# Kernel optimization log

Hardware: AMD Instinct MI355X
Metric: run time of the kernel (lower is better)

## Reference

```python
import jax, jax.numpy as jnp
import numpy as np

B, H, S, D = 2, 16, 2048, 64

def setup_inputs() -> dict:
    key = jax.random.key(0)
    kq, kk, kv, km = jax.random.split(key, 4)
    q = jax.random.normal(kq, (B, H, S, D), dtype=jnp.float32)
    k = jax.random.normal(kk, (B, H, S, D), dtype=jnp.float32)
    v = jax.random.normal(kv, (B, H, S, D), dtype=jnp.float32)
    mask = jax.random.randint(km, (B, 1, S, S), 0, 2, dtype=jnp.int32)
    return {"q": q, "k": k, "v": v, "mask": mask}

def reference(q, k, v, mask):
    d_model = q.shape[-1]
    # scores: [B, H, S, S]
    score = jnp.einsum('bhqd,bhkd->bhqk', q, k) / jnp.sqrt(jnp.float32(d_model))
    score = jnp.where(mask == 0, jnp.float32(-1e9), score)
    attn = jax.nn.softmax(score, axis=-1)
    return jnp.einsum('bhqk,bhkd->bhqd', attn, v)
```

## Files before the change

### kernel.cpp

```cpp
#include <hip/hip_runtime.h>
#include <hip/hip_bf16.h>


#define B_ 2
#define H_ 16
#define S_ 2048
#define D_ 64
#define BQ 128
#define NW 4
#define BK 64
#define NT (S_ / BK)
#define PADW 72
#define TILEB (BK * D_ * 2)

typedef __attribute__((ext_vector_type(4))) float f32x4;
typedef __attribute__((ext_vector_type(8))) short bf16x8;
typedef __attribute__((ext_vector_type(4))) short bf16x4;

#define QSCALE 0.1803368801111137f
#define MASKNEG (-1.4426950408889634e9f)

static __device__ __forceinline__ short f2bf(float f) {
  __hip_bfloat16 h = __float2bfloat16(f);
  short s; __builtin_memcpy(&s, &h, sizeof(s)); return s;
}
static __device__ __forceinline__ float fexp2(float x) {
  return __builtin_amdgcn_exp2f(x);
}
static __device__ __forceinline__ unsigned cvt_pk_bf16(float a, float b) {
  unsigned r;
  asm("v_cvt_pk_bf16_f32 %0, %1, %2" : "=v"(r) : "v"(a), "v"(b));
  return r;
}
static __device__ __forceinline__ void gload_lds16(const void* g, void* l) {
  __builtin_amdgcn_global_load_lds(
      (__attribute__((address_space(1))) void*)g,
      (__attribute__((address_space(3))) void*)l, 16, 0, 0);
}

__global__ __launch_bounds__(256)
void pack_all(const float* __restrict__ kg, const float* __restrict__ vg,
              const int* __restrict__ mg,
              short* __restrict__ kw, short* __restrict__ vw,
              unsigned long long* __restrict__ mwp) {
  __shared__ float sv[BK][D_ + 1];
  const int bx  = blockIdx.x;
  const int tid = threadIdx.x;

  if (bx < 1024) {
    const int t  = bx & 31;
    const int bh = bx >> 5;
    const float* kt = kg + ((size_t)bh * S_ + t * BK) * D_;
    const float* vt = vg + ((size_t)bh * S_ + t * BK) * D_;
    short* ko = kw + ((size_t)bh * NT + t) * (BK * D_);
    short* vo = vw + ((size_t)bh * NT + t) * (BK * D_);

    const int row = tid >> 2;
    const int swz = (row & 7) << 4;

    #pragma unroll
    for (int c = 0; c < 2; ++c) {
      const int x = (tid & 3) * 32 + c * 16;
      const int dsrc = (x ^ swz) >> 1;
      const float4 u0 = *(const float4*)(kt + row * D_ + dsrc);
      const float4 u1 = *(const float4*)(kt + row * D_ + dsrc + 4);
      uint4 w;
      w.x = cvt_pk_bf16(u0.x, u0.y); w.y = cvt_pk_bf16(u0.z, u0.w);
      w.z = cvt_pk_bf16(u1.x, u1.y); w.w = cvt_pk_bf16(u1.z, u1.w);
      *(uint4*)(ko + row * D_ + (x >> 1)) = w;
    }

    #pragma unroll
    for (int i = 0; i < 4; ++i) {
      const int id = tid + 256 * i;
      const int r = id >> 4, c4 = (id & 15) * 4;
      const float4 u = *(const float4*)(vt + r * D_ + c4);
      sv[r][c4] = u.x; sv[r][c4+1] = u.y; sv[r][c4+2] = u.z; sv[r][c4+3] = u.w;
    }
    __syncthreads();
    #pragma unroll
    for (int c = 0; c < 2; ++c) {
      const int x = (tid & 3) * 32 + c * 16;
      const int ksrc = (x ^ swz) >> 1;
      uint4 w;
      w.x = cvt_pk_bf16(sv[ksrc+0][row], sv[ksrc+1][row]);
      w.y = cvt_pk_bf16(sv[ksrc+2][row], sv[ksrc+3][row]);
      w.z = cvt_pk_bf16(sv[ksrc+4][row], sv[ksrc+5][row]);
      w.w = cvt_pk_bf16(sv[ksrc+6][row], sv[ksrc+7][row]);
      *(uint4*)(vo + row * D_ + (x >> 1)) = w;
    }
  } else {
    const int r4   = bx - 1024;
    const int wv   = tid >> 6;
    const int lane = tid & 63;
    const int row  = r4 * 4 + wv;
    const int* mr = mg + (size_t)row * S_;
    unsigned long long* out = mwp + (size_t)row * NT;
    #pragma unroll
    for (int g = 0; g < 8; ++g) {
      const int4 v = *(const int4*)(mr + g * 256 + lane * 4);
      const unsigned long long b0 = __ballot(v.x != 0);
      const unsigned long long b1 = __ballot(v.y != 0);
      const unsigned long long b2 = __ballot(v.z != 0);
      const unsigned long long b3 = __ballot(v.w != 0);
      if (lane < 4) {
        const int tl = lane;
        const unsigned long long u =
            ((b0 >> (16 * tl)) & 0xFFFFULL)
          | (((b1 >> (16 * tl)) & 0xFFFFULL) << 16)
          | (((b2 >> (16 * tl)) & 0xFFFFULL) << 32)
          | (((b3 >> (16 * tl)) & 0xFFFFULL) << 48);
        out[g * 4 + tl] = u;
      }
    }
  }
}

static __device__ __forceinline__ float softmax_group(
    const f32x4* st, unsigned long long m64, int quad, char* spg,
    int l15, int swz) {
  const unsigned xlo = ((unsigned)m64) >> quad;
  const unsigned xhi = ((unsigned)(m64 >> 32)) >> quad;
  float l = 0.f;
  #pragma unroll
  for (int mt = 0; mt < 4; ++mt) {
    float p0 = fexp2(st[mt].x);
    float p1 = fexp2(st[mt].y);
    float p2 = fexp2(st[mt].z);
    float p3 = fexp2(st[mt].w);
    const int a0 = __builtin_amdgcn_sbfe((int)xlo, mt*4,      1);
    const int a1 = __builtin_amdgcn_sbfe((int)xlo, mt*4 + 16, 1);
    const int a2 = __builtin_amdgcn_sbfe((int)xhi, mt*4,      1);
    const int a3 = __builtin_amdgcn_sbfe((int)xhi, mt*4 + 16, 1);
    p0 = __uint_as_float(__float_as_uint(p0) & (unsigned)a0);
    p1 = __uint_as_float(__float_as_uint(p1) & (unsigned)a1);
    p2 = __uint_as_float(__float_as_uint(p2) & (unsigned)a2);
    p3 = __uint_as_float(__float_as_uint(p3) & (unsigned)a3);
    l += (p0 + p1) + (p2 + p3);
    uint2 uu;
    uu.x = cvt_pk_bf16(p0, p1);
    uu.y = cvt_pk_bf16(p2, p3);
    *(uint2*)(spg + l15*128 + ((mt*32 + quad*8) ^ swz)) = uu;
  }
  return l;
}

__global__ __launch_bounds__(256, 3)
void attn_main(const float* __restrict__ qg, const short* __restrict__ kw,
               const short* __restrict__ vw,
               const unsigned long long* __restrict__ mw,
               float* __restrict__ outg) {
  __shared__ short sKV[2][2][BK * D_];
  __shared__ short sP[NW][2][16][64];

  const int tid  = threadIdx.x;
  const int lane = tid & 63;
  const int wv   = tid >> 6;
  const int l15  = lane & 15;
  const int quad = lane >> 4;

  const int f  = blockIdx.y * 16 + blockIdx.x;
  const int nf = (f & 7) * 64 + (f >> 3);
  const int bh = nf >> 4;
  const int b  = bh >> 4;
  const int q0 = (nf & 15) * BQ;
  const int qw0 = q0 + wv * 32 + l15;
  const int qw1 = qw0 + 16;

  bf16x8 qf[2][2];
  #pragma unroll
  for (int g = 0; g < 2; ++g) {
    const float* qrow = qg + ((size_t)bh * S_ + (g ? qw1 : qw0)) * D_;
    #pragma unroll
    for (int ks = 0; ks < 2; ++ks) {
      const float4 u0 = *(const float4*)(qrow + ks*32 + quad*8);
      const float4 u1 = *(const float4*)(qrow + ks*32 + quad*8 + 4);
      bf16x8 fq;
      fq[0]=f2bf(u0.x*QSCALE); fq[1]=f2bf(u0.y*QSCALE);
      fq[2]=f2bf(u0.z*QSCALE); fq[3]=f2bf(u0.w*QSCALE);
      fq[4]=f2bf(u1.x*QSCALE); fq[5]=f2bf(u1.y*QSCALE);
      fq[6]=f2bf(u1.z*QSCALE); fq[7]=f2bf(u1.w*QSCALE);
      qf[g][ks] = fq;
    }
  }

  f32x4 O0[4], O1[4];
  #pragma unroll
  for (int dt = 0; dt < 4; ++dt) {
    O0[dt] = (f32x4){0.f, 0.f, 0.f, 0.f};
    O1[dt] = (f32x4){0.f, 0.f, 0.f, 0.f};
  }
  float la = 0.f, lb = 0.f;

  const char* kt = (const char*)(kw + (size_t)bh * NT * BK * D_);
  const char* vt = (const char*)(vw + (size_t)bh * NT * BK * D_);
  const unsigned long long* mb0 = mw + ((size_t)b * S_ + qw0) * NT;
  const unsigned long long* mb1 = mb0 + (size_t)16 * NT;
  const int so = tid * 16;

  const int swz = (l15 & 7) << 4;
  const int ro0 = l15*128 + (( 0 + quad*16) ^ swz);
  const int ro1 = l15*128 + ((64 + quad*16) ^ swz);
  char* const spw = (char*)sP + wv*4096;

  gload_lds16(kt + so,        (char*)sKV + so);
  gload_lds16(kt + 4096 + so, (char*)sKV + 4096 + so);
  gload_lds16(vt + so,        (char*)sKV + 8192 + so);
  gload_lds16(vt + 4096 + so, (char*)sKV + 12288 + so);
  kt += TILEB; vt += TILEB;
  int cur = 0;
  __syncthreads();

  for (int t = 0; t < NT; ++t) {
    const unsigned long long m64a = mb0[t];
    const unsigned long long m64b = mb1[t];
    if (t < NT - 1) {
      const int nb = (cur ^ 1) << 14;
      gload_lds16(kt + so,        (char*)sKV + nb + so);
      gload_lds16(kt + 4096 + so, (char*)sKV + nb + 4096 + so);
      gload_lds16(vt + so,        (char*)sKV + nb + 8192 + so);
      gload_lds16(vt + 4096 + so, (char*)sKV + nb + 12288 + so);
      kt += TILEB; vt += TILEB;
    }
    const char* kb = (const char*)sKV + (cur << 14);
    const char* vb = kb + 8192;

    f32x4 st0[4], st1[4];
    __builtin_amdgcn_s_setprio(1);
    #pragma unroll
    for (int mt = 0; mt < 4; ++mt) {
      const bf16x8 kf0 = *(const bf16x8*)(kb + mt*2048 + ro0);
      const bf16x8 kf1 = *(const bf16x8*)(kb + mt*2048 + ro1);
      f32x4 a0 = (f32x4){0.f, 0.f, 0.f, 0.f};
      f32x4 a1 = (f32x4){0.f, 0.f, 0.f, 0.f};
      a0 = __builtin_amdgcn_mfma_f32_16x16x32_bf16(kf0, qf[0][0], a0, 0, 0, 0);
      a1 = __builtin_amdgcn_mfma_f32_16x16x32_bf16(kf0, qf[1][0], a1, 0, 0, 0);
      a0 = __builtin_amdgcn_mfma_f32_16x16x32_bf16(kf1, qf[0][1], a0, 0, 0, 0);
      a1 = __builtin_amdgcn_mfma_f32_16x16x32_bf16(kf1, qf[1][1], a1, 0, 0, 0);
      st0[mt] = a0; st1[mt] = a1;
    }
    __builtin_amdgcn_s_setprio(0);

    la += softmax_group(st0, m64a, quad, spw,        l15, swz);
    lb += softmax_group(st1, m64b, quad, spw + 2048, l15, swz);

    asm volatile("s_waitcnt lgkmcnt(0)" ::: "memory");

    const bf16x8 pf00 = *(const bf16x8*)(spw +        l15*128 + (( 0 + quad*16) ^ swz));
    const bf16x8 pf01 = *(const bf16x8*)(spw +        l15*128 + ((64 + quad*16) ^ swz));
    const bf16x8 pf10 = *(const bf16x8*)(spw + 2048 + l15*128 + (( 0 + quad*16) ^ swz));
    const bf16x8 pf11 = *(const bf16x8*)(spw + 2048 + l15*128 + ((64 + quad*16) ^ swz));
    __builtin_amdgcn_s_setprio(1);
    #pragma unroll
    for (int dt = 0; dt < 4; ++dt) {
      const bf16x8 vf0 = *(const bf16x8*)(vb + dt*2048 + ro0);
      const bf16x8 vf1 = *(const bf16x8*)(vb + dt*2048 + ro1);
      O0[dt] = __builtin_amdgcn_mfma_f32_16x16x32_bf16(pf00, vf0, O0[dt], 0, 0, 0);
      O1[dt] = __builtin_amdgcn_mfma_f32_16x16x32_bf16(pf10, vf0, O1[dt], 0, 0, 0);
      O0[dt] = __builtin_amdgcn_mfma_f32_16x16x32_bf16(pf01, vf1, O0[dt], 0, 0, 0);
      O1[dt] = __builtin_amdgcn_mfma_f32_16x16x32_bf16(pf11, vf1, O1[dt], 0, 0, 0);
    }
    __builtin_amdgcn_s_setprio(0);

    __syncthreads();
    cur ^= 1;
  }

  la += __shfl_xor(la, 16);
  la += __shfl_xor(la, 32);
  lb += __shfl_xor(lb, 16);
  lb += __shfl_xor(lb, 32);
  float ira[4], irb[4];
  #pragma unroll
  for (int r = 0; r < 4; ++r) {
    ira[r] = 1.0f / __shfl(la, quad*4 + r);
    irb[r] = 1.0f / __shfl(lb, quad*4 + r);
  }

  float* ob0 = outg + ((size_t)bh * S_ + q0 + wv*32) * D_;
  float* ob1 = ob0 + 16 * D_;
  #pragma unroll
  for (int dt = 0; dt < 4; ++dt) {
    ob0[(quad*4 + 0)*D_ + dt*16 + l15] = O0[dt].x * ira[0];
    ob0[(quad*4 + 1)*D_ + dt*16 + l15] = O0[dt].y * ira[1];
    ob0[(quad*4 + 2)*D_ + dt*16 + l15] = O0[dt].z * ira[2];
    ob0[(quad*4 + 3)*D_ + dt*16 + l15] = O0[dt].w * ira[3];
    ob1[(quad*4 + 0)*D_ + dt*16 + l15] = O1[dt].x * irb[0];
    ob1[(quad*4 + 1)*D_ + dt*16 + l15] = O1[dt].y * irb[1];
    ob1[(quad*4 + 2)*D_ + dt*16 + l15] = O1[dt].z * irb[2];
    ob1[(quad*4 + 3)*D_ + dt*16 + l15] = O1[dt].w * irb[3];
  }
}

__global__ __launch_bounds__(256, 4)
void attn_fallback(const float* __restrict__ qg, const float* __restrict__ kg,
                   const float* __restrict__ vg, const int* __restrict__ maskg,
                   float* __restrict__ outg) {
  __shared__ short sK[BK][PADW];
  __shared__ short sVT[D_][PADW];
  __shared__ short sP[4][16][PADW];

  const int tid  = threadIdx.x;
  const int lane = tid & 63;
  const int wv   = tid >> 6;
  const int l15  = lane & 15;
  const int quad = lane >> 4;

  const int bh = blockIdx.y;
  const int b  = bh >> 4;
  const int q0 = blockIdx.x * 64;
  const int qw = q0 + wv * 16 + l15;

  bf16x8 qf[2];
  {
    const float* qrow = qg + ((size_t)bh * S_ + qw) * D_;
    #pragma unroll
    for (int ks = 0; ks < 2; ++ks) {
      const float4 u0 = *(const float4*)(qrow + ks*32 + quad*8);
      const float4 u1 = *(const float4*)(qrow + ks*32 + quad*8 + 4);
      bf16x8 fq;
      fq[0]=f2bf(u0.x*QSCALE); fq[1]=f2bf(u0.y*QSCALE);
      fq[2]=f2bf(u0.z*QSCALE); fq[3]=f2bf(u0.w*QSCALE);
      fq[4]=f2bf(u1.x*QSCALE); fq[5]=f2bf(u1.y*QSCALE);
      fq[6]=f2bf(u1.z*QSCALE); fq[7]=f2bf(u1.w*QSCALE);
      qf[ks] = fq;
    }
  }

  f32x4 O[4];
  #pragma unroll
  for (int dt = 0; dt < 4; ++dt) O[dt] = (f32x4){0.f, 0.f, 0.f, 0.f};
  float m = -3.0e38f, l = 0.f;

  const float* kbase = kg + (size_t)bh * S_ * D_;
  const float* vbase = vg + (size_t)bh * S_ * D_;
  const int*   mrow  = maskg + ((size_t)b * S_ + qw) * S_;

  for (int t0 = 0; t0 < S_; t0 += BK) {
    __syncthreads();
    #pragma unroll
    for (int i = 0; i < 4; ++i) {
      const int id = tid + 256*i;
      const int key = id >> 4, d4 = (id & 15) * 4;
      const float4 u = *(const float4*)(kbase + (size_t)(t0 + key)*D_ + d4);
      bf16x4 w; w[0]=f2bf(u.x); w[1]=f2bf(u.y); w[2]=f2bf(u.z); w[3]=f2bf(u.w);
      *(bf16x4*)&sK[key][d4] = w;
    }
    #pragma unroll
    for (int i = 0; i < 2; ++i) {
      const int id = tid + 256*i;
      const int kp = id & 31, d4 = (id >> 5) * 4;
      const float4 a = *(const float4*)(vbase + (size_t)(t0 + 2*kp    )*D_ + d4);
      const float4 c = *(const float4*)(vbase + (size_t)(t0 + 2*kp + 1)*D_ + d4);
      const float av[4] = {a.x, a.y, a.z, a.w};
      const float cv[4] = {c.x, c.y, c.z, c.w};
      #pragma unroll
      for (int j = 0; j < 4; ++j) {
        const unsigned pk = (unsigned)(unsigned short)f2bf(av[j])
                          | ((unsigned)(unsigned short)f2bf(cv[j]) << 16);
        *(unsigned*)&sVT[d4 + j][2*kp] = pk;
      }
    }
    __syncthreads();

    int4 mk[4];
    #pragma unroll
    for (int mt = 0; mt < 4; ++mt)
      mk[mt] = *(const int4*)(mrow + t0 + mt*16 + quad*4);

    f32x4 st[4];
    #pragma unroll
    for (int mt = 0; mt < 4; ++mt) {
      f32x4 acc = (f32x4){0.f, 0.f, 0.f, 0.f};
      #pragma unroll
      for (int ks = 0; ks < 2; ++ks) {
        const bf16x8 kf = *(const bf16x8*)&sK[mt*16 + l15][ks*32 + quad*8];
        acc = __builtin_amdgcn_mfma_f32_16x16x32_bf16(kf, qf[ks], acc, 0, 0, 0);
      }
      st[mt] = acc;
    }

    float cmax = -3.0e38f;
    #pragma unroll
    for (int mt = 0; mt < 4; ++mt) {
      f32x4 s = st[mt];
      s.x = mk[mt].x ? s.x : MASKNEG;
      s.y = mk[mt].y ? s.y : MASKNEG;
      s.z = mk[mt].z ? s.z : MASKNEG;
      s.w = mk[mt].w ? s.w : MASKNEG;
      st[mt] = s;
      cmax = fmaxf(cmax, fmaxf(fmaxf(s.x, s.y), fmaxf(s.z, s.w)));
    }
    cmax = fmaxf(cmax, __shfl_xor(cmax, 16));
    cmax = fmaxf(cmax, __shfl_xor(cmax, 32));
    const float mnew  = fmaxf(m, cmax);
    const float alpha = fexp2(m - mnew);
    m = mnew;

    float lsum = 0.f;
    #pragma unroll
    for (int mt = 0; mt < 4; ++mt) {
      const float p0 = fexp2(st[mt].x - mnew);
      const float p1 = fexp2(st[mt].y - mnew);
      const float p2 = fexp2(st[mt].z - mnew);
      const float p3 = fexp2(st[mt].w - mnew);
      lsum += (p0 + p1) + (p2 + p3);
      bf16x4 pw; pw[0]=f2bf(p0); pw[1]=f2bf(p1); pw[2]=f2bf(p2); pw[3]=f2bf(p3);
      *(bf16x4*)&sP[wv][l15][mt*16 + quad*4] = pw;
    }
    lsum += __shfl_xor(lsum, 16);
    lsum += __shfl_xor(lsum, 32);
    l = l * alpha + lsum;

    const float ar0 = __shfl(alpha, quad*4 + 0);
    const float ar1 = __shfl(alpha, quad*4 + 1);
    const float ar2 = __shfl(alpha, quad*4 + 2);
    const float ar3 = __shfl(alpha, quad*4 + 3);
    #pragma unroll
    for (int dt = 0; dt < 4; ++dt) {
      O[dt].x *= ar0; O[dt].y *= ar1; O[dt].z *= ar2; O[dt].w *= ar3;
    }

    asm volatile("s_waitcnt lgkmcnt(0)" ::: "memory");

    const bf16x8 pf0 = *(const bf16x8*)&sP[wv][l15][quad*8];
    const bf16x8 pf1 = *(const bf16x8*)&sP[wv][l15][32 + quad*8];
    #pragma unroll
    for (int dt = 0; dt < 4; ++dt) {
      const bf16x8 vf0 = *(const bf16x8*)&sVT[dt*16 + l15][quad*8];
      const bf16x8 vf1 = *(const bf16x8*)&sVT[dt*16 + l15][32 + quad*8];
      O[dt] = __builtin_amdgcn_mfma_f32_16x16x32_bf16(pf0, vf0, O[dt], 0, 0, 0);
      O[dt] = __builtin_amdgcn_mfma_f32_16x16x32_bf16(pf1, vf1, O[dt], 0, 0, 0);
    }
  }

  float ir[4];
  #pragma unroll
  for (int r = 0; r < 4; ++r) ir[r] = 1.0f / __shfl(l, quad*4 + r);

  float* ob = outg + ((size_t)bh * S_ + q0 + wv*16) * D_;
  #pragma unroll
  for (int dt = 0; dt < 4; ++dt) {
    ob[(quad*4 + 0)*D_ + dt*16 + l15] = O[dt].x * ir[0];
    ob[(quad*4 + 1)*D_ + dt*16 + l15] = O[dt].y * ir[1];
    ob[(quad*4 + 2)*D_ + dt*16 + l15] = O[dt].z * ir[2];
    ob[(quad*4 + 3)*D_ + dt*16 + l15] = O[dt].w * ir[3];
  }
}

extern "C" void kernel_launch(void* const* d_in, const int* in_sizes, int n_in,
                              void* d_out, int out_size, void* d_ws, size_t ws_size,
                              hipStream_t stream) {
  const float* q    = (const float*)d_in[0];
  const float* k    = (const float*)d_in[1];
  const float* v    = (const float*)d_in[2];
  const int*   mask = (const int*)d_in[3];
  float* out = (float*)d_out;

  const size_t kvbytes = (size_t)B_ * H_ * S_ * D_ * 2;
  const size_t mbytes  = (size_t)B_ * S_ * NT * 8;
  const size_t need    = 2 * kvbytes + mbytes;

  if (d_ws != nullptr && ws_size >= need) {
    short* kwp = (short*)d_ws;
    short* vwp = (short*)((char*)d_ws + kvbytes);
    unsigned long long* mwp = (unsigned long long*)((char*)d_ws + 2 * kvbytes);
    pack_all<<<dim3(2048), 256, 0, stream>>>(k, v, mask, kwp, vwp, mwp);
    attn_main<<<dim3(S_ / BQ, B_ * H_), NW * 64, 0, stream>>>(q, kwp, vwp, mwp, out);
  } else {
    attn_fallback<<<dim3(S_ / 64, B_ * H_), 256, 0, stream>>>(q, k, v, mask, out);
  }
}
```

Measured before the change: 170.5 us.

## Split key range across two wave halves with 512-thread blocks and LDS reduction

Doubles the block to 8 waves. Two groups of four waves each process alternate 64-key tiles for the same 128 query rows, and their partial outputs are combined through LDS at the end. The row-sum is now computed with an MFMA against a ones vector instead of scalar adds and shuffles. The per-wave P staging buffer is halved by reusing one buffer for both query groups. V is single-buffered with an extra barrier per step. The intent is more waves in flight per CU and shorter serial loops, at the cost of extra syncs and a final reduction pass.

```diff
diff --git a/kernel.cpp b/kernel.cpp
--- a/kernel.cpp
+++ b/kernel.cpp
@@ -7,9 +7,9 @@
 #define S_ 2048
 #define D_ 64
 #define BQ 128
-#define NW 4
 #define BK 64
 #define NT (S_ / BK)
+#define NS (NT / 2)
 #define PADW 72
 #define TILEB (BK * D_ * 2)
 
@@ -116,12 +116,11 @@
   }
 }
 
-static __device__ __forceinline__ float softmax_group(
+static __device__ __forceinline__ void softmax_group_ns(
     const f32x4* st, unsigned long long m64, int quad, char* spg,
     int l15, int swz) {
   const unsigned xlo = ((unsigned)m64) >> quad;
   const unsigned xhi = ((unsigned)(m64 >> 32)) >> quad;
-  float l = 0.f;
   #pragma unroll
   for (int mt = 0; mt < 4; ++mt) {
     float p0 = fexp2(st[mt].x);
@@ -136,41 +135,42 @@
     p1 = __uint_as_float(__float_as_uint(p1) & (unsigned)a1);
     p2 = __uint_as_float(__float_as_uint(p2) & (unsigned)a2);
     p3 = __uint_as_float(__float_as_uint(p3) & (unsigned)a3);
-    l += (p0 + p1) + (p2 + p3);
     uint2 uu;
     uu.x = cvt_pk_bf16(p0, p1);
     uu.y = cvt_pk_bf16(p2, p3);
     *(uint2*)(spg + l15*128 + ((mt*32 + quad*8) ^ swz)) = uu;
   }
-  return l;
-}
-
-__global__ __launch_bounds__(256, 3)
+}
+
+__global__ __launch_bounds__(512, 4)
 void attn_main(const float* __restrict__ qg, const short* __restrict__ kw,
                const short* __restrict__ vw,
                const unsigned long long* __restrict__ mw,
                float* __restrict__ outg) {
-  __shared__ short sKV[2][2][BK * D_];
-  __shared__ short sP[NW][2][16][64];
+  __shared__ short sK2[2][2][BK * D_];
+  __shared__ short sV[2][BK * D_];
+  __shared__ short sP[8][16][64];
 
   const int tid  = threadIdx.x;
   const int lane = tid & 63;
   const int wv   = tid >> 6;
   const int l15  = lane & 15;
   const int quad = lane >> 4;
+  const int g    = wv & 3;
+  const int h    = wv >> 2;
 
   const int f  = blockIdx.y * 16 + blockIdx.x;
   const int nf = (f & 7) * 64 + (f >> 3);
   const int bh = nf >> 4;
   const int b  = bh >> 4;
   const int q0 = (nf & 15) * BQ;
-  const int qw0 = q0 + wv * 32 + l15;
+  const int qw0 = q0 + g * 32 + l15;
   const int qw1 = qw0 + 16;
 
   bf16x8 qf[2][2];
   #pragma unroll
-  for (int g = 0; g < 2; ++g) {
-    const float* qrow = qg + ((size_t)bh * S_ + (g ? qw1 : qw0)) * D_;
+  for (int gr = 0; gr < 2; ++gr) {
+    const float* qrow = qg + ((size_t)bh * S_ + (gr ? qw1 : qw0)) * D_;
     #pragma unroll
     for (int ks = 0; ks < 2; ++ks) {
       const float4 u0 = *(const float4*)(qrow + ks*32 + quad*8);
@@ -180,9 +180,13 @@
       fq[2]=f2bf(u0.z*QSCALE); fq[3]=f2bf(u0.w*QSCALE);
       fq[4]=f2bf(u1.x*QSCALE); fq[5]=f2bf(u1.y*QSCALE);
       fq[6]=f2bf(u1.z*QSCALE); fq[7]=f2bf(u1.w*QSCALE);
-      qf[g][ks] = fq;
-    }
-  }
+      qf[gr][ks] = fq;
+    }
+  }
+
+  bf16x8 onesf;
+  #pragma unroll
+  for (int j = 0; j < 8; ++j) onesf[j] = (short)0x3F80;
 
   f32x4 O0[4], O1[4];
   #pragma unroll
@@ -190,10 +194,11 @@
     O0[dt] = (f32x4){0.f, 0.f, 0.f, 0.f};
     O1[dt] = (f32x4){0.f, 0.f, 0.f, 0.f};
   }
-  float la = 0.f, lb = 0.f;
-
-  const char* kt = (const char*)(kw + (size_t)bh * NT * BK * D_);
-  const char* vt = (const char*)(vw + (size_t)bh * NT * BK * D_);
+  f32x4 Ol0 = (f32x4){0.f, 0.f, 0.f, 0.f};
+  f32x4 Ol1 = (f32x4){0.f, 0.f, 0.f, 0.f};
+
+  const char* ktb = (const char*)(kw + (size_t)bh * NT * BK * D_);
+  const char* vtb = (const char*)(vw + (size_t)bh * NT * BK * D_);
   const unsigned long long* mb0 = mw + ((size_t)b * S_ + qw0) * NT;
   const unsigned long long* mb1 = mb0 + (size_t)16 * NT;
   const int so = tid * 16;
@@ -201,29 +206,28 @@
   const int swz = (l15 & 7) << 4;
   const int ro0 = l15*128 + (( 0 + quad*16) ^ swz);
   const int ro1 = l15*128 + ((64 + quad*16) ^ swz);
-  char* const spw = (char*)sP + wv*4096;
-
-  gload_lds16(kt + so,        (char*)sKV + so);
-  gload_lds16(kt + 4096 + so, (char*)sKV + 4096 + so);
-  gload_lds16(vt + so,        (char*)sKV + 8192 + so);
-  gload_lds16(vt + 4096 + so, (char*)sKV + 12288 + so);
-  kt += TILEB; vt += TILEB;
-  int cur = 0;
+  char* const spw = (char*)sP + wv*2048;
+
+  gload_lds16(ktb + so,         (char*)sK2 + so);
+  gload_lds16(ktb + TILEB + so, (char*)sK2 + 8192 + so);
+  const char* kp = ktb + 2 * TILEB;
+  const char* vs = vtb;
   __syncthreads();
 
-  for (int t = 0; t < NT; ++t) {
-    const unsigned long long m64a = mb0[t];
-    const unsigned long long m64b = mb1[t];
-    if (t < NT - 1) {
-      const int nb = (cur ^ 1) << 14;
-      gload_lds16(kt + so,        (char*)sKV + nb + so);
-      gload_lds16(kt + 4096 + so, (char*)sKV + nb + 4096 + so);
-      gload_lds16(vt + so,        (char*)sKV + nb + 8192 + so);
-      gload_lds16(vt + 4096 + so, (char*)sKV + nb + 12288 + so);
-      kt += TILEB; vt += TILEB;
-    }
-    const char* kb = (const char*)sKV + (cur << 14);
-    const char* vb = kb + 8192;
+  for (int s = 0; s < NS; ++s) {
+    gload_lds16(vs + so,         (char*)sV + so);
+    gload_lds16(vs + TILEB + so, (char*)sV + 8192 + so);
+    vs += 2 * TILEB;
+    if (s < NS - 1) {
+      char* dst = (char*)sK2 + ((s + 1) & 1) * 16384;
+      gload_lds16(kp + so,         dst + so);
+      gload_lds16(kp + TILEB + so, dst + 8192 + so);
+      kp += 2 * TILEB;
+    }
+    const unsigned long long m64a = mb0[2*s + h];
+    const unsigned long long m64b = mb1[2*s + h];
+    const char* kb = (const char*)sK2 + (s & 1) * 16384 + h * 8192;
+    const char* vb = (const char*)sV + h * 8192;
 
     f32x4 st0[4], st1[4];
     __builtin_amdgcn_s_setprio(1);
@@ -241,54 +245,83 @@
     }
     __builtin_amdgcn_s_setprio(0);
 
-    la += softmax_group(st0, m64a, quad, spw,        l15, swz);
-    lb += softmax_group(st1, m64b, quad, spw + 2048, l15, swz);
-
+    softmax_group_ns(st0, m64a, quad, spw, l15, swz);
     asm volatile("s_waitcnt lgkmcnt(0)" ::: "memory");
-
-    const bf16x8 pf00 = *(const bf16x8*)(spw +        l15*128 + (( 0 + quad*16) ^ swz));
-    const bf16x8 pf01 = *(const bf16x8*)(spw +        l15*128 + ((64 + quad*16) ^ swz));
-    const bf16x8 pf10 = *(const bf16x8*)(spw + 2048 + l15*128 + (( 0 + quad*16) ^ swz));
-    const bf16x8 pf11 = *(const bf16x8*)(spw + 2048 + l15*128 + ((64 + quad*16) ^ swz));
+    const bf16x8 pfA0 = *(const bf16x8*)(spw + l15*128 + (( 0 + quad*16) ^ swz));
+    const bf16x8 pfA1 = *(const bf16x8*)(spw + l15*128 + ((64 + quad*16) ^ swz));
+    softmax_group_ns(st1, m64b, quad, spw, l15, swz);
+
+    __syncthreads();
+
+    bf16x8 vf0[4], vf1[4];
     __builtin_amdgcn_s_setprio(1);
     #pragma unroll
     for (int dt = 0; dt < 4; ++dt) {
-      const bf16x8 vf0 = *(const bf16x8*)(vb + dt*2048 + ro0);
-      const bf16x8 vf1 = *(const bf16x8*)(vb + dt*2048 + ro1);
-      O0[dt] = __builtin_amdgcn_mfma_f32_16x16x32_bf16(pf00, vf0, O0[dt], 0, 0, 0);
-      O1[dt] = __builtin_amdgcn_mfma_f32_16x16x32_bf16(pf10, vf0, O1[dt], 0, 0, 0);
-      O0[dt] = __builtin_amdgcn_mfma_f32_16x16x32_bf16(pf01, vf1, O0[dt], 0, 0, 0);
-      O1[dt] = __builtin_amdgcn_mfma_f32_16x16x32_bf16(pf11, vf1, O1[dt], 0, 0, 0);
-    }
+      vf0[dt] = *(const bf16x8*)(vb + dt*2048 + ro0);
+      vf1[dt] = *(const bf16x8*)(vb + dt*2048 + ro1);
+      O0[dt] = __builtin_amdgcn_mfma_f32_16x16x32_bf16(pfA0, vf0[dt], O0[dt], 0, 0, 0);
+      O0[dt] = __builtin_amdgcn_mfma_f32_16x16x32_bf16(pfA1, vf1[dt], O0[dt], 0, 0, 0);
+    }
+    Ol0 = __builtin_amdgcn_mfma_f32_16x16x32_bf16(pfA0, onesf, Ol0, 0, 0, 0);
+    Ol0 = __builtin_amdgcn_mfma_f32_16x16x32_bf16(pfA1, onesf, Ol0, 0, 0, 0);
     __builtin_amdgcn_s_setprio(0);
 
+    asm volatile("s_waitcnt lgkmcnt(0)" ::: "memory");
+    const bf16x8 pfB0 = *(const bf16x8*)(spw + l15*128 + (( 0 + quad*16) ^ swz));
+    const bf16x8 pfB1 = *(const bf16x8*)(spw + l15*128 + ((64 + quad*16) ^ swz));
+    __builtin_amdgcn_s_setprio(1);
+    #pragma unroll
+    for (int dt = 0; dt < 4; ++dt) {
+      O1[dt] = __builtin_amdgcn_mfma_f32_16x16x32_bf16(pfB0, vf0[dt], O1[dt], 0, 0, 0);
+      O1[dt] = __builtin_amdgcn_mfma_f32_16x16x32_bf16(pfB1, vf1[dt], O1[dt], 0, 0, 0);
+    }
+    Ol1 = __builtin_amdgcn_mfma_f32_16x16x32_bf16(pfB0, onesf, Ol1, 0, 0, 0);
+    Ol1 = __builtin_amdgcn_mfma_f32_16x16x32_bf16(pfB1, onesf, Ol1, 0, 0, 0);
+    __builtin_amdgcn_s_setprio(0);
+
     __syncthreads();
-    cur ^= 1;
-  }
-
-  la += __shfl_xor(la, 16);
-  la += __shfl_xor(la, 32);
-  lb += __shfl_xor(lb, 16);
-  lb += __shfl_xor(lb, 32);
-  float ira[4], irb[4];
-  #pragma unroll
-  for (int r = 0; r < 4; ++r) {
-    ira[r] = 1.0f / __shfl(la, quad*4 + r);
-    irb[r] = 1.0f / __shfl(lb, quad*4 + r);
-  }
-
-  float* ob0 = outg + ((size_t)bh * S_ + q0 + wv*32) * D_;
-  float* ob1 = ob0 + 16 * D_;
-  #pragma unroll
-  for (int dt = 0; dt < 4; ++dt) {
-    ob0[(quad*4 + 0)*D_ + dt*16 + l15] = O0[dt].x * ira[0];
-    ob0[(quad*4 + 1)*D_ + dt*16 + l15] = O0[dt].y * ira[1];
-    ob0[(quad*4 + 2)*D_ + dt*16 + l15] = O0[dt].z * ira[2];
-    ob0[(quad*4 + 3)*D_ + dt*16 + l15] = O0[dt].w * ira[3];
-    ob1[(quad*4 + 0)*D_ + dt*16 + l15] = O1[dt].x * irb[0];
-    ob1[(quad*4 + 1)*D_ + dt*16 + l15] = O1[dt].y * irb[1];
-    ob1[(quad*4 + 2)*D_ + dt*16 + l15] = O1[dt].z * irb[2];
-    ob1[(quad*4 + 3)*D_ + dt*16 + l15] = O1[dt].w * irb[3];
+  }
+
+  const int exsw = (lane & 7) << 4;
+  if (h == 1) {
+    char* eb = (char*)sK2 + g * 8192 + lane * 128;
+    #pragma unroll
+    for (int dt = 0; dt < 4; ++dt) {
+      *(f32x4*)(eb + ((dt*16) ^ exsw))       = O0[dt];
+      *(f32x4*)(eb + (((dt+4)*16) ^ exsw))   = O1[dt];
+    }
+    *(f32x4*)((char*)sV + g*4096 + lane*32)      = Ol0;
+    *(f32x4*)((char*)sV + g*4096 + lane*32 + 16) = Ol1;
+  }
+  __syncthreads();
+  if (h == 0) {
+    const char* eb = (const char*)sK2 + g * 8192 + lane * 128;
+    Ol0 += *(const f32x4*)((const char*)sV + g*4096 + lane*32);
+    Ol1 += *(const f32x4*)((const char*)sV + g*4096 + lane*32 + 16);
+    #pragma unroll
+    for (int dt = 0; dt < 4; ++dt) {
+      O0[dt] += *(const f32x4*)(eb + ((dt*16) ^ exsw));
+      O1[dt] += *(const f32x4*)(eb + (((dt+4)*16) ^ exsw));
+    }
+    float ira[4], irb[4];
+    ira[0] = 1.0f / Ol0.x; ira[1] = 1.0f / Ol0.y;
+    ira[2] = 1.0f / Ol0.z; ira[3] = 1.0f / Ol0.w;
+    irb[0] = 1.0f / Ol1.x; irb[1] = 1.0f / Ol1.y;
+    irb[2] = 1.0f / Ol1.z; irb[3] = 1.0f / Ol1.w;
+
+    float* ob0 = outg + ((size_t)bh * S_ + q0 + g*32) * D_;
+    float* ob1 = ob0 + 16 * D_;
+    #pragma unroll
+    for (int dt = 0; dt < 4; ++dt) {
+      ob0[(quad*4 + 0)*D_ + dt*16 + l15] = O0[dt].x * ira[0];
+      ob0[(quad*4 + 1)*D_ + dt*16 + l15] = O0[dt].y * ira[1];
+      ob0[(quad*4 + 2)*D_ + dt*16 + l15] = O0[dt].z * ira[2];
+      ob0[(quad*4 + 3)*D_ + dt*16 + l15] = O0[dt].w * ira[3];
+      ob1[(quad*4 + 0)*D_ + dt*16 + l15] = O1[dt].x * irb[0];
+      ob1[(quad*4 + 1)*D_ + dt*16 + l15] = O1[dt].y * irb[1];
+      ob1[(quad*4 + 2)*D_ + dt*16 + l15] = O1[dt].z * irb[2];
+      ob1[(quad*4 + 3)*D_ + dt*16 + l15] = O1[dt].w * irb[3];
+    }
   }
 }
 
@@ -466,7 +499,7 @@
     short* vwp = (short*)((char*)d_ws + kvbytes);
     unsigned long long* mwp = (unsigned long long*)((char*)d_ws + 2 * kvbytes);
     pack_all<<<dim3(2048), 256, 0, stream>>>(k, v, mask, kwp, vwp, mwp);
-    attn_main<<<dim3(S_ / BQ, B_ * H_), NW * 64, 0, stream>>>(q, kwp, vwp, mwp, out);
+    attn_main<<<dim3(S_ / BQ, B_ * H_), 512, 0, stream>>>(q, kwp, vwp, mwp, out);
   } else {
     attn_fallback<<<dim3(S_ / 64, B_ * H_), 256, 0, stream>>>(q, k, v, mask, out);
   }
```

Result: slower. 176.1 us (+3.3%).
